# Performance work log

Hardware: AMD Instinct MI355X
Metric: run time of the kernel (lower is better)

## Reference

```python
import jax, jax.numpy as jnp
import numpy as np

N_NODES = 100_000
N_EDGES = 1_600_000
D_IN = 128
D_HID = 128
D_OUT = 128
N_GRAPHS = 1024


def setup_inputs() -> dict:
    key = jax.random.key(0)
    ks = jax.random.split(key, 7)
    x = jax.random.normal(ks[0], (N_NODES, D_IN), dtype=jnp.float32)
    edge_index = jax.random.randint(ks[1], (2, N_EDGES), 0, N_NODES, dtype=jnp.int32)
    batch = jnp.sort(jax.random.randint(ks[2], (N_NODES,), 0, N_GRAPHS, dtype=jnp.int32))
    W1 = jax.random.normal(ks[3], (D_IN, D_HID), dtype=jnp.float32) * (1.0 / np.sqrt(D_IN))
    b1 = jax.random.normal(ks[4], (D_HID,), dtype=jnp.float32) * 0.01
    W2 = jax.random.normal(ks[5], (D_HID, D_OUT), dtype=jnp.float32) * (1.0 / np.sqrt(D_HID))
    b2 = jax.random.normal(ks[6], (D_OUT,), dtype=jnp.float32) * 0.01
    return {"x": x, "edge_index": edge_index, "batch": batch,
            "W1": W1, "b1": b1, "W2": W2, "b2": b2, "num_graphs": N_GRAPHS}


def gcn_conv(x, edge_index, W, b):
    """PyG GCNConv: add self-loops, symmetric deg^{-1/2} norm, linear, scatter-add."""
    n = x.shape[0]
    xw = x @ W  # [N, H] -- transform before propagate, as PyG does
    loop = jnp.arange(n, dtype=edge_index.dtype)
    src = jnp.concatenate([edge_index[0], loop])  # message source (x_j)
    dst = jnp.concatenate([edge_index[1], loop])  # aggregation target
    deg = jax.ops.segment_sum(jnp.ones_like(dst, dtype=xw.dtype), dst, num_segments=n)
    dinv = jnp.where(deg > 0, jax.lax.rsqrt(deg), 0.0)
    norm = dinv[src] * dinv[dst]  # [E+N]
    out = jax.ops.segment_sum(norm[:, None] * xw[src], dst, num_segments=n)
    return out + b


def reference(x, edge_index, batch, W1, b1, W2, b2, num_graphs):
    h = jax.nn.relu(gcn_conv(x, edge_index, W1, b1))
    h = gcn_conv(h, edge_index, W2, b2)
    # global_mean_pool over graph ids
    s = jax.ops.segment_sum(h, batch, num_segments=num_graphs)          # [G, D_OUT]
    cnt = jax.ops.segment_sum(jnp.ones((x.shape[0],), h.dtype), batch, num_segments=num_graphs)
    return s / jnp.maximum(cnt, 1.0)[:, None]
```

## Files before the change

kernel.cpp:

```cpp
#include <hip/hip_runtime.h>

constexpr int D = 128;
constexpr int PAD = 48;
constexpr int EBLK = 4096;
constexpr int WNODE = 256;
constexpr int CAPW = 32;
constexpr int SCAP = 8192;

typedef __attribute__((ext_vector_type(8))) short short8;
typedef __attribute__((ext_vector_type(4))) float floatx4;
typedef __attribute__((ext_vector_type(2))) float floatx2;
typedef unsigned short ushort_t;
typedef unsigned char uchar_t;

static inline size_t ws_align(size_t x) { return (x + 255) & ~size_t(255); }

__device__ inline unsigned pack_bf16(float a, float b) {
  unsigned ua = __float_as_uint(a), ub = __float_as_uint(b);
  ua += 0x7fffu + ((ua >> 16) & 1u);
  ub += 0x7fffu + ((ub >> 16) & 1u);
  return ((ua >> 16) & 0xffffu) | (ub & 0xffff0000u);
}
__device__ inline ushort_t f32_to_bf16u(float f) {
  unsigned u = __float_as_uint(f);
  u += 0x7fffu + ((u >> 16) & 1u);
  return (ushort_t)(u >> 16);
}
__device__ inline float bf16u_to_f32(ushort_t u) {
  return __uint_as_float(((unsigned)u) << 16);
}
__device__ inline uchar_t f32_to_fp8(float v) {
  int p = __builtin_amdgcn_cvt_pk_fp8_f32(v, v, 0, false);
  return (uchar_t)(p & 0xff);
}
__device__ inline void fp8x4_acc(unsigned u, float* v) {
  floatx2 a = __builtin_amdgcn_cvt_pk_f32_fp8((int)u, false);
  floatx2 b = __builtin_amdgcn_cvt_pk_f32_fp8((int)u, true);
  v[0] += a.x; v[1] += a.y; v[2] += b.x; v[3] += b.y;
}
__device__ inline void fp8x4_acc2(unsigned u, floatx2* v) {
  v[0] += __builtin_amdgcn_cvt_pk_f32_fp8((int)u, false);
  v[1] += __builtin_amdgcn_cvt_pk_f32_fp8((int)u, true);
}

__global__ __launch_bounds__(256) void k_prep(
    const int* __restrict__ src, const int* __restrict__ dst, int E,
    int nstrips, int nw,
    unsigned* __restrict__ bucket, int* __restrict__ bkcnt,
    uint2* __restrict__ spill, int* __restrict__ scnt,
    const float* __restrict__ W1, const float* __restrict__ W2,
    ushort_t* __restrict__ w1t, ushort_t* __restrict__ w2t, int nbin) {
  const int b = blockIdx.x;
  const int t = threadIdx.x;
  if (b < nbin) {
    __shared__ int lcnt[512];
    for (int i = t; i < nw; i += 256) lcnt[i] = 0;
    __syncthreads();
    const int base = b * EBLK;
    const int end = min(base + EBLK, E);
    for (int j = base + t; j < end; j += 256) {
      int ss = src[j], dd = dst[j];
      int wnd = dd >> 8;
      unsigned pk = ((unsigned)(dd & 255) << 17) | (unsigned)ss;
      int p = atomicAdd(&lcnt[wnd], 1);
      if (p < CAPW) {
        bucket[((size_t)wnd * nstrips + b) * CAPW + p] = pk;
      } else {
        int sp = atomicAdd(scnt, 1);
        if (sp < SCAP) spill[sp] = make_uint2((unsigned)ss, (unsigned)dd);
      }
    }
    __syncthreads();
    for (int i = t; i < nw; i += 256)
      bkcnt[(size_t)i * nstrips + b] = min(lcnt[i], CAPW);
    return;
  }
  {
    int idx = (b - nbin) * 256 + t;
    int k = idx >> 7, n = idx & 127;
    w1t[n * 128 + k] = f32_to_bf16u(W1[idx]);
    w2t[n * 128 + k] = f32_to_bf16u(W2[idx]);
  }
}

__global__ __launch_bounds__(256) void k_fill(
    const unsigned* __restrict__ bucket, const int* __restrict__ bkcnt,
    const uint2* __restrict__ spill, const int* __restrict__ scnt,
    int* __restrict__ cnt, int* __restrict__ csrp, int N, int nstrips) {
  __shared__ int lc[WNODE];
  __shared__ int ls[WNODE * PAD];
  const int w = blockIdx.x;
  const int t = threadIdx.x;
  const int wbase = w << 8;
  const int nn = min(WNODE, N - wbase);
  for (int i = t; i < WNODE; i += 256) lc[i] = 0;
  __syncthreads();
  const int* bc = bkcnt + (size_t)w * nstrips;
  for (int sb = t; sb < nstrips; sb += 256) {
    int c = bc[sb];
    const uint4* bk4 = (const uint4*)(bucket + ((size_t)w * nstrips + sb) * CAPW);
    int c4 = (c + 3) >> 2;
    for (int j4 = 0; j4 < c4; ++j4) {
      uint4 v = bk4[j4];
      unsigned e[4] = {v.x, v.y, v.z, v.w};
#pragma unroll
      for (int u = 0; u < 4; ++u) {
        int j = j4 * 4 + u;
        if (j < c) {
          unsigned pk = e[u];
          int dl = (int)(pk >> 17);
          int p = atomicAdd(&lc[dl], 1);
          if (p < PAD) ls[dl * PAD + p] = (int)(pk & 0x1FFFFu);
        }
      }
    }
  }
  {
    int ns = min(*scnt, SCAP);
    for (int j = t; j < ns; j += 256) {
      uint2 e = spill[j];
      if ((int)(e.y >> 8) == w) {
        int dl = (int)(e.y & 255u);
        int p = atomicAdd(&lc[dl], 1);
        if (p < PAD) ls[dl * PAD + p] = (int)e.x;
      }
    }
  }
  __syncthreads();
  const int total = nn * PAD;
  int4* dp = (int4*)(csrp + (size_t)wbase * PAD);
  const int4* sp = (const int4*)ls;
  for (int i = t; i < (total >> 2); i += 256) dp[i] = sp[i];
  for (int i = (total & ~3) + t; i < total; i += 256)
    csrp[(size_t)wbase * PAD + i] = ls[i];
  for (int i = t; i < nn; i += 256) cnt[wbase + i] = lc[i];
}

template <bool A_FP32>
__global__ __launch_bounds__(256) void k_gemm(
    const void* __restrict__ Av, const ushort_t* __restrict__ Wt,
    const int* __restrict__ cnt, uchar_t* __restrict__ Y, int N) {
  __shared__ ushort_t As[128 * 128];
  __shared__ ushort_t Bs[128 * 128];
  const int t = threadIdx.x;
  const int rowBase = blockIdx.x * 128;

  {
    const uint4* g = (const uint4*)Wt;
#pragma unroll
    for (int i = 0; i < 8; ++i) {
      int idx = t + 256 * i;
      int r = idx >> 4, c = idx & 15;
      int cs = c ^ (r & 15);
      *(uint4*)&Bs[r * 128 + cs * 8] = g[idx];
    }
  }
  if (A_FP32) {
    const float4* A = (const float4*)Av;
#pragma unroll
    for (int i = 0; i < 16; ++i) {
      int idx = t + 256 * i;
      int r = idx >> 5, c4 = idx & 31;
      int grow = rowBase + r;
      float4 v = make_float4(0.f, 0.f, 0.f, 0.f);
      if (grow < N) v = A[(size_t)grow * 32 + c4];
      int cs = (c4 >> 1) ^ (r & 15);
      unsigned* p = (unsigned*)&As[r * 128 + cs * 8 + (c4 & 1) * 4];
      p[0] = pack_bf16(v.x, v.y);
      p[1] = pack_bf16(v.z, v.w);
    }
  } else {
    const uint4* A = (const uint4*)Av;
#pragma unroll
    for (int i = 0; i < 8; ++i) {
      int idx = t + 256 * i;
      int r = idx >> 4, c = idx & 15;
      int grow = rowBase + r;
      uint4 v = make_uint4(0u, 0u, 0u, 0u);
      if (grow < N) v = A[(size_t)grow * 16 + c];
      int cs = c ^ (r & 15);
      *(uint4*)&As[r * 128 + cs * 8] = v;
    }
  }
  __syncthreads();

  const int w = t >> 6;
  const int l = t & 63;
  const int qd = l >> 4, lm = l & 15;
  const int mrow = w * 32;

  floatx4 acc[2][8];
#pragma unroll
  for (int i = 0; i < 2; ++i)
#pragma unroll
    for (int j = 0; j < 8; ++j) acc[i][j] = (floatx4){0.f, 0.f, 0.f, 0.f};

#pragma unroll
  for (int ks = 0; ks < 4; ++ks) {
    const int ch = ks * 4 + qd;
    const int chs = ch ^ lm;
    short8 a0 = *(const short8*)&As[(mrow + lm) * 128 + chs * 8];
    short8 a1 = *(const short8*)&As[(mrow + 16 + lm) * 128 + chs * 8];
#pragma unroll
    for (int j = 0; j < 8; ++j) {
      short8 b = *(const short8*)&Bs[(j * 16 + lm) * 128 + chs * 8];
      acc[0][j] = __builtin_amdgcn_mfma_f32_16x16x32_bf16(a0, b, acc[0][j], 0, 0, 0);
      acc[1][j] = __builtin_amdgcn_mfma_f32_16x16x32_bf16(a1, b, acc[1][j], 0, 0, 0);
    }
  }

  float s[2][4];
#pragma unroll
  for (int i = 0; i < 2; ++i)
#pragma unroll
    for (int r = 0; r < 4; ++r) {
      int grow = rowBase + mrow + i * 16 + qd * 4 + r;
      s[i][r] = (grow < N) ? rsqrtf(1.f + (float)cnt[grow]) : 0.f;
    }
#pragma unroll
  for (int i = 0; i < 2; ++i)
#pragma unroll
    for (int j = 0; j < 8; ++j)
#pragma unroll
      for (int r = 0; r < 4; ++r) {
        int grow = rowBase + mrow + i * 16 + qd * 4 + r;
        if (grow < N)
          Y[(size_t)grow * 128 + j * 16 + lm] = f32_to_fp8(s[i][r] * acc[i][j][r]);
      }
}

template <bool RELU>
__global__ __launch_bounds__(256) void k_aggregate(
    const uchar_t* __restrict__ y, const int* __restrict__ csrp,
    const int* __restrict__ cnt, const float* __restrict__ bias,
    ushort_t* __restrict__ out, int N) {
  const int wid = threadIdx.x >> 6;
  const int n0 = blockIdx.x * 8 + wid * 2;
  if (n0 >= N) return;
  const int n1 = n0 + 1;
  const bool hasB = (n1 < N);
  const int l = threadIdx.x & 63;
  const int eg = l >> 4, q = l & 15;
  const uint2* yb = (const uint2*)y;
  int degA0 = cnt[n0];
  int degB0 = hasB ? cnt[n1] : 0;
  float dvA = rsqrtf(1.f + (float)degA0);
  float dvB = rsqrtf(1.f + (float)degB0);
  int degA = degA0 > PAD ? PAD : degA0;
  int degB = degB0 > PAD ? PAD : degB0;
  int idxA = 0, idxB = 0;
  if (l < PAD) {
    idxA = csrp[(size_t)n0 * PAD + l];
    if (hasB) idxB = csrp[(size_t)n1 * PAD + l];
  }
  uint2 sv = make_uint2(0u, 0u);
  if (eg == 0) sv = yb[(size_t)n0 * 16 + q];
  else if (eg == 1 && hasB) sv = yb[(size_t)n1 * 16 + q];
  floatx2 vA[4], vB[4];
#pragma unroll
  for (int k = 0; k < 4; ++k) { vA[k] = (floatx2){0.f, 0.f}; vB[k] = (floatx2){0.f, 0.f}; }
  const int dmax = degA > degB ? degA : degB;
  const int iters = (dmax + 15) >> 4;
  for (int it = 0; it < iters; ++it) {
    int p0 = it * 16 + eg;
    int p1 = p0 + 4, p2 = p0 + 8, p3 = p0 + 12;
    int a0 = __shfl(idxA, p0);
    int a1 = __shfl(idxA, p1);
    int a2 = __shfl(idxA, p2);
    int a3 = __shfl(idxA, p3);
    int b0 = __shfl(idxB, p0);
    int b1 = __shfl(idxB, p1);
    int b2 = __shfl(idxB, p2);
    int b3 = __shfl(idxB, p3);
    if (p0 < degA) { uint2 v = yb[(size_t)a0 * 16 + q]; fp8x4_acc2(v.x, vA); fp8x4_acc2(v.y, vA + 2); }
    if (p0 < degB) { uint2 v = yb[(size_t)b0 * 16 + q]; fp8x4_acc2(v.x, vB); fp8x4_acc2(v.y, vB + 2); }
    if (p1 < degA) { uint2 v = yb[(size_t)a1 * 16 + q]; fp8x4_acc2(v.x, vA); fp8x4_acc2(v.y, vA + 2); }
    if (p1 < degB) { uint2 v = yb[(size_t)b1 * 16 + q]; fp8x4_acc2(v.x, vB); fp8x4_acc2(v.y, vB + 2); }
    if (p2 < degA) { uint2 v = yb[(size_t)a2 * 16 + q]; fp8x4_acc2(v.x, vA); fp8x4_acc2(v.y, vA + 2); }
    if (p2 < degB) { uint2 v = yb[(size_t)b2 * 16 + q]; fp8x4_acc2(v.x, vB); fp8x4_acc2(v.y, vB + 2); }
    if (p3 < degA) { uint2 v = yb[(size_t)a3 * 16 + q]; fp8x4_acc2(v.x, vA); fp8x4_acc2(v.y, vA + 2); }
    if (p3 < degB) { uint2 v = yb[(size_t)b3 * 16 + q]; fp8x4_acc2(v.x, vB); fp8x4_acc2(v.y, vB + 2); }
  }
  float fA[8] = {vA[0].x, vA[0].y, vA[1].x, vA[1].y, vA[2].x, vA[2].y, vA[3].x, vA[3].y};
  float fB[8] = {vB[0].x, vB[0].y, vB[1].x, vB[1].y, vB[2].x, vB[2].y, vB[3].x, vB[3].y};
#pragma unroll
  for (int k = 0; k < 8; ++k) {
    fA[k] += __shfl_xor(fA[k], 32); fA[k] += __shfl_xor(fA[k], 16);
    fB[k] += __shfl_xor(fB[k], 32); fB[k] += __shfl_xor(fB[k], 16);
  }
  if (eg == 0 || (eg == 1 && hasB)) {
    float dv = (eg == 0) ? dvA : dvB;
    int node = (eg == 0) ? n0 : n1;
    float f[8];
#pragma unroll
    for (int k = 0; k < 8; ++k) f[k] = (eg == 0) ? fA[k] : fB[k];
    fp8x4_acc(sv.x, f); fp8x4_acc(sv.y, f + 4);
    float4 c0 = ((const float4*)bias)[2 * q];
    float4 c1 = ((const float4*)bias)[2 * q + 1];
    float o[8];
    o[0] = dv * f[0] + c0.x; o[1] = dv * f[1] + c0.y;
    o[2] = dv * f[2] + c0.z; o[3] = dv * f[3] + c0.w;
    o[4] = dv * f[4] + c1.x; o[5] = dv * f[5] + c1.y;
    o[6] = dv * f[6] + c1.z; o[7] = dv * f[7] + c1.w;
    if (RELU) {
#pragma unroll
      for (int k = 0; k < 8; ++k) o[k] = fmaxf(o[k], 0.f);
    }
    uint4 pk;
    pk.x = pack_bf16(o[0], o[1]); pk.y = pack_bf16(o[2], o[3]);
    pk.z = pack_bf16(o[4], o[5]); pk.w = pack_bf16(o[6], o[7]);
    ((uint4*)out)[(size_t)node * 16 + q] = pk;
  }
}

__global__ __launch_bounds__(512) void k_pool(
    const ushort_t* __restrict__ h, const int* __restrict__ batch,
    float* __restrict__ out, int N, int G) {
  __shared__ float part[4][128];
  int g = blockIdx.x;
  int col = threadIdx.x & 127;
  int pr = threadIdx.x >> 7;
  int lo = 0, hi = N;
  while (lo < hi) { int m = (lo + hi) >> 1; if (batch[m] < g) lo = m + 1; else hi = m; }
  int start = lo;
  hi = N;
  while (lo < hi) { int m = (lo + hi) >> 1; if (batch[m] <= g) lo = m + 1; else hi = m; }
  int end = lo;
  float sum = 0.f;
  for (int r = start + pr; r < end; r += 4) sum += bf16u_to_f32(h[(size_t)r * D + col]);
  part[pr][col] = sum;
  __syncthreads();
  if (pr == 0) {
    float s = part[0][col] + part[1][col] + part[2][col] + part[3][col];
    int c = end - start;
    out[(size_t)g * D + col] = s / (float)(c > 0 ? c : 1);
  }
}

extern "C" void kernel_launch(void* const* d_in, const int* in_sizes, int n_in,
                              void* d_out, int out_size, void* d_ws, size_t ws_size,
                              hipStream_t stream) {
  const float* x  = (const float*)d_in[0];
  const int* edge = (const int*)d_in[1];
  const int* batch = (const int*)d_in[2];
  const float* W1 = (const float*)d_in[3];
  const float* b1 = (const float*)d_in[4];
  const float* W2 = (const float*)d_in[5];
  const float* b2 = (const float*)d_in[6];
  float* out = (float*)d_out;

  const int N = in_sizes[0] / D;
  const int E = in_sizes[1] / 2;
  const int G = out_size / D;
  const int* esrc = edge;
  const int* edst = edge + E;

  const int nstrips = (E + EBLK - 1) / EBLK;
  const int nw = (N + WNODE - 1) / WNODE;

  char* ws = (char*)d_ws;
  size_t off = 0;
  auto alloc = [&](size_t bytes) {
    char* p = ws + off;
    off = ws_align(off + bytes);
    return p;
  };
  uchar_t* bufY = (uchar_t*)alloc((size_t)N * D);
  ushort_t* bufH = (ushort_t*)alloc((size_t)N * D * 2);
  int* cnt = (int*)alloc((size_t)N * 4);
  int* csrp = (int*)alloc((size_t)N * PAD * 4);
  ushort_t* w1t = (ushort_t*)alloc((size_t)D * D * 2);
  ushort_t* w2t = (ushort_t*)alloc((size_t)D * D * 2);
  unsigned* bucket = (unsigned*)alloc((size_t)nw * nstrips * CAPW * 4);
  int* bkcnt = (int*)alloc((size_t)nw * nstrips * 4);
  uint2* spill = (uint2*)alloc((size_t)SCAP * 8);
  int* scnt = (int*)alloc(256);

  const int tb = 256;

  hipMemsetAsync(scnt, 0, 4, stream);

  const int nbin = nstrips;
  const int nwp = (D * D) / 256;
  k_prep<<<nbin + nwp, tb, 0, stream>>>(esrc, edst, E, nstrips, nw,
                                        bucket, bkcnt, spill, scnt,
                                        W1, W2, w1t, w2t, nbin);

  k_fill<<<nw, tb, 0, stream>>>(bucket, bkcnt, spill, scnt, cnt, csrp, N, nstrips);

  const int gblk = (N + 127) / 128;
  const int ablk = (N + 7) / 8;
  k_gemm<true><<<gblk, 256, 0, stream>>>(x, w1t, cnt, bufY, N);
  k_aggregate<true><<<ablk, 256, 0, stream>>>(bufY, csrp, cnt, b1, bufH, N);
  k_gemm<false><<<gblk, 256, 0, stream>>>(bufH, w2t, cnt, bufY, N);
  k_aggregate<false><<<ablk, 256, 0, stream>>>(bufY, csrp, cnt, b2, bufH, N);
  k_pool<<<G, 512, 0, stream>>>(bufH, batch, out, N, G);
}
```

Baseline: 279.9 us.

## Widen GEMM blocks to 512 threads and parallelize bucket reads across lanes in fill

k_fill now assigns one strip to each group of 8 lanes, with every lane loading a single uint4 of that strip's bucket. Previously one thread walked a whole strip serially, so this gives coalesced, more parallel loads and less per-thread serialization. The GEMM kernel moves to 512 threads per 128-row tile, with each wave computing 16 rows instead of 32. This halves the per-thread load and accumulator work and gives more waves for latency hiding, at the cost of less B-fragment reuse per wave and higher LDS-limited occupancy pressure.

```diff
diff --git a/kernel.cpp b/kernel.cpp
--- a/kernel.cpp
+++ b/kernel.cpp
@@ -96,22 +96,25 @@
   for (int i = t; i < WNODE; i += 256) lc[i] = 0;
   __syncthreads();
   const int* bc = bkcnt + (size_t)w * nstrips;
-  for (int sb = t; sb < nstrips; sb += 256) {
-    int c = bc[sb];
-    const uint4* bk4 = (const uint4*)(bucket + ((size_t)w * nstrips + sb) * CAPW);
-    int c4 = (c + 3) >> 2;
-    for (int j4 = 0; j4 < c4; ++j4) {
-      uint4 v = bk4[j4];
-      unsigned e[4] = {v.x, v.y, v.z, v.w};
-#pragma unroll
-      for (int u = 0; u < 4; ++u) {
-        int j = j4 * 4 + u;
-        if (j < c) {
-          unsigned pk = e[u];
-          int dl = (int)(pk >> 17);
-          int p = atomicAdd(&lc[dl], 1);
-          if (p < PAD) ls[dl * PAD + p] = (int)(pk & 0x1FFFFu);
-        }
+  const unsigned* bwin = bucket + (size_t)w * nstrips * CAPW;
+  const int wid = t >> 6, l = t & 63;
+  const int sgrp = l >> 3;
+  const int ui = l & 7;
+  for (int sb0 = wid * 8; sb0 < nstrips; sb0 += 32) {
+    int s = sb0 + sgrp;
+    int c = (s < nstrips) ? bc[s] : 0;
+    uint4 v = make_uint4(0u, 0u, 0u, 0u);
+    if (ui * 4 < c)
+      v = ((const uint4*)(bwin + (size_t)s * CAPW))[ui];
+    unsigned e[4] = {v.x, v.y, v.z, v.w};
+#pragma unroll
+    for (int u = 0; u < 4; ++u) {
+      int j = ui * 4 + u;
+      if (j < c) {
+        unsigned pk = e[u];
+        int dl = (int)(pk >> 17);
+        int p = atomicAdd(&lc[dl], 1);
+        if (p < PAD) ls[dl * PAD + p] = (int)(pk & 0x1FFFFu);
       }
     }
   }
@@ -137,7 +140,7 @@
 }
 
 template <bool A_FP32>
-__global__ __launch_bounds__(256) void k_gemm(
+__global__ __launch_bounds__(512) void k_gemm(
     const void* __restrict__ Av, const ushort_t* __restrict__ Wt,
     const int* __restrict__ cnt, uchar_t* __restrict__ Y, int N) {
   __shared__ ushort_t As[128 * 128];
@@ -148,8 +151,8 @@
   {
     const uint4* g = (const uint4*)Wt;
 #pragma unroll
-    for (int i = 0; i < 8; ++i) {
-      int idx = t + 256 * i;
+    for (int i = 0; i < 4; ++i) {
+      int idx = t + 512 * i;
       int r = idx >> 4, c = idx & 15;
       int cs = c ^ (r & 15);
       *(uint4*)&Bs[r * 128 + cs * 8] = g[idx];
@@ -158,8 +161,8 @@
   if (A_FP32) {
     const float4* A = (const float4*)Av;
 #pragma unroll
-    for (int i = 0; i < 16; ++i) {
-      int idx = t + 256 * i;
+    for (int i = 0; i < 8; ++i) {
+      int idx = t + 512 * i;
       int r = idx >> 5, c4 = idx & 31;
       int grow = rowBase + r;
       float4 v = make_float4(0.f, 0.f, 0.f, 0.f);
@@ -172,8 +175,8 @@
   } else {
     const uint4* A = (const uint4*)Av;
 #pragma unroll
-    for (int i = 0; i < 8; ++i) {
-      int idx = t + 256 * i;
+    for (int i = 0; i < 4; ++i) {
+      int idx = t + 512 * i;
       int r = idx >> 4, c = idx & 15;
       int grow = rowBase + r;
       uint4 v = make_uint4(0u, 0u, 0u, 0u);
@@ -187,46 +190,38 @@
   const int w = t >> 6;
   const int l = t & 63;
   const int qd = l >> 4, lm = l & 15;
-  const int mrow = w * 32;
-
-  floatx4 acc[2][8];
-#pragma unroll
-  for (int i = 0; i < 2; ++i)
-#pragma unroll
-    for (int j = 0; j < 8; ++j) acc[i][j] = (floatx4){0.f, 0.f, 0.f, 0.f};
+  const int mrow = w * 16;
+
+  floatx4 acc[8];
+#pragma unroll
+  for (int j = 0; j < 8; ++j) acc[j] = (floatx4){0.f, 0.f, 0.f, 0.f};
 
 #pragma unroll
   for (int ks = 0; ks < 4; ++ks) {
     const int ch = ks * 4 + qd;
     const int chs = ch ^ lm;
     short8 a0 = *(const short8*)&As[(mrow + lm) * 128 + chs * 8];
-    short8 a1 = *(const short8*)&As[(mrow + 16 + lm) * 128 + chs * 8];
 #pragma unroll
     for (int j = 0; j < 8; ++j) {
       short8 b = *(const short8*)&Bs[(j * 16 + lm) * 128 + chs * 8];
-      acc[0][j] = __builtin_amdgcn_mfma_f32_16x16x32_bf16(a0, b, acc[0][j], 0, 0, 0);
-      acc[1][j] = __builtin_amdgcn_mfma_f32_16x16x32_bf16(a1, b, acc[1][j], 0, 0, 0);
-    }
-  }
-
-  float s[2][4];
-#pragma unroll
-  for (int i = 0; i < 2; ++i)
+      acc[j] = __builtin_amdgcn_mfma_f32_16x16x32_bf16(a0, b, acc[j], 0, 0, 0);
+    }
+  }
+
+  float s[4];
+#pragma unroll
+  for (int r = 0; r < 4; ++r) {
+    int grow = rowBase + mrow + qd * 4 + r;
+    s[r] = (grow < N) ? rsqrtf(1.f + (float)cnt[grow]) : 0.f;
+  }
+#pragma unroll
+  for (int j = 0; j < 8; ++j)
 #pragma unroll
     for (int r = 0; r < 4; ++r) {
-      int grow = rowBase + mrow + i * 16 + qd * 4 + r;
-      s[i][r] = (grow < N) ? rsqrtf(1.f + (float)cnt[grow]) : 0.f;
-    }
-#pragma unroll
-  for (int i = 0; i < 2; ++i)
-#pragma unroll
-    for (int j = 0; j < 8; ++j)
-#pragma unroll
-      for (int r = 0; r < 4; ++r) {
-        int grow = rowBase + mrow + i * 16 + qd * 4 + r;
-        if (grow < N)
-          Y[(size_t)grow * 128 + j * 16 + lm] = f32_to_fp8(s[i][r] * acc[i][j][r]);
-      }
+      int grow = rowBase + mrow + qd * 4 + r;
+      if (grow < N)
+        Y[(size_t)grow * 128 + j * 16 + lm] = f32_to_fp8(s[r] * acc[j][r]);
+    }
 }
 
 template <bool RELU>
@@ -390,9 +385,9 @@
 
   const int gblk = (N + 127) / 128;
   const int ablk = (N + 7) / 8;
-  k_gemm<true><<<gblk, 256, 0, stream>>>(x, w1t, cnt, bufY, N);
+  k_gemm<true><<<gblk, 512, 0, stream>>>(x, w1t, cnt, bufY, N);
   k_aggregate<true><<<ablk, 256, 0, stream>>>(bufY, csrp, cnt, b1, bufH, N);
-  k_gemm<false><<<gblk, 256, 0, stream>>>(bufH, w2t, cnt, bufY, N);
+  k_gemm<false><<<gblk, 512, 0, stream>>>(bufH, w2t, cnt, bufY, N);
   k_aggregate<false><<<ablk, 256, 0, stream>>>(bufY, csrp, cnt, b2, bufH, N);
   k_pool<<<G, 512, 0, stream>>>(bufH, batch, out, N, G);
 }
```

Measured after the change: 265.4 us. 1.05x faster.
